# Kernel tuning notes

Hardware: AMD Instinct MI355X
Metric: run time of the kernel (lower is better)

## Reference

```python
import jax, jax.numpy as jnp
import numpy as np

N = 100000          # nodes
E = 1600000         # edges
IN, H, E1, E2, K = 256, 128, 128, 128, 3


def setup_inputs() -> dict:
    key = jax.random.key(0)
    ks = jax.random.split(key, 8)
    s = 0.02
    return {
        "x": jax.random.normal(ks[0], (N, IN), dtype=jnp.float32),
        "edge_index": jax.random.randint(ks[1], (2, E), 0, N),
        "edge_weight": jax.random.uniform(ks[2], (E,), dtype=jnp.float32),
        "W1": jax.random.normal(ks[3], (IN, H), dtype=jnp.float32) * s,
        "b1": jnp.zeros((H,), jnp.float32),
        "cheb1_W": jax.random.normal(ks[4], (K, H, E1), dtype=jnp.float32) * s,
        "cheb1_b": jnp.zeros((E1,), jnp.float32),
        "cheb2_W": jax.random.normal(ks[5], (K, E1, E2), dtype=jnp.float32) * s,
        "cheb2_b": jnp.zeros((E2,), jnp.float32),
        "W2": jax.random.normal(ks[6], (E2, 2), dtype=jnp.float32) * s,
        "b2": jnp.zeros((2,), jnp.float32),
    }


def _cheb_conv(x, row, col, wn, Ws, b):
    """PyG ChebConv with sym normalization, lambda_max=2.
    Scaled Laplacian L_hat = L_sym - I = -D^{-1/2} A D^{-1/2} (zero diagonal),
    so L_hat @ v is a single gather/scale/scatter over edges.
    Tx_0 = x; Tx_1 = L_hat x; Tx_k = 2 L_hat Tx_{k-1} - Tx_{k-2}.
    """
    n = x.shape[0]

    def Lx(v):
        return jax.ops.segment_sum(-wn[:, None] * v[col], row, num_segments=n)

    Tx0 = x
    out = Tx0 @ Ws[0]
    Tx1 = Lx(Tx0)
    out = out + Tx1 @ Ws[1]
    for k in range(2, Ws.shape[0]):
        Tx2 = 2.0 * Lx(Tx1) - Tx0
        out = out + Tx2 @ Ws[k]
        Tx0, Tx1 = Tx1, Tx2
    return out + b


def reference(x, edge_index, edge_weight, W1, b1, cheb1_W, cheb1_b,
              cheb2_W, cheb2_b, W2, b2):
    row, col = edge_index[0], edge_index[1]
    n = x.shape[0]
    # symmetric normalization of edge weights (shared by both convs)
    deg = jax.ops.segment_sum(edge_weight, row, num_segments=n)
    safe = jnp.where(deg > 0, deg, 1.0)
    dinv = jnp.where(deg > 0, jax.lax.rsqrt(safe), 0.0)
    wn = dinv[row] * edge_weight * dinv[col]

    # dropout is identity in eval mode
    h = jax.nn.relu(x @ W1 + b1)
    h = jax.nn.relu(_cheb_conv(h, row, col, wn, cheb1_W, cheb1_b))
    h = jax.nn.relu(_cheb_conv(h, row, col, wn, cheb2_W, cheb2_b))
    logits = h @ W2 + b2
    return jax.nn.softmax(logits, axis=1)
```

## Files before the change

kernel.cpp:

```cpp
#include <hip/hip_runtime.h>
#include <hip/hip_bf16.h>
#include <stdint.h>

typedef __bf16 bf16_t;
typedef __bf16 bf16x8 __attribute__((ext_vector_type(8)));
typedef float f32x4 __attribute__((ext_vector_type(4)));
typedef float f32x2 __attribute__((ext_vector_type(2)));
typedef float floatv4 __attribute__((ext_vector_type(4)));

static __device__ __forceinline__ float bflo(unsigned int p){ return __uint_as_float(p << 16); }
static __device__ __forceinline__ float bfhi(unsigned int p){ return __uint_as_float(p & 0xffff0000u); }
static __device__ __forceinline__ unsigned int pack2(float lo, float hi){
  union { bf16_t h[2]; unsigned int u; } o;
  o.h[0] = (bf16_t)lo; o.h[1] = (bf16_t)hi;
  return o.u;
}
static __device__ __forceinline__ void gload16(const void* g, void* l){
  __builtin_amdgcn_global_load_lds((const __attribute__((address_space(1))) void*)g,
                                   (__attribute__((address_space(3))) void*)l, 16, 0, 0);
}
static __device__ __forceinline__ void acc4_fp8(float* a, unsigned w, float wt){
  f32x2 lo, hi;
  unsigned wh = w >> 16;
  asm("v_cvt_pk_f32_fp8 %0, %1" : "=v"(lo) : "v"(w));
  asm("v_cvt_pk_f32_fp8 %0, %1" : "=v"(hi) : "v"(wh));
  a[0] += wt*lo[0]; a[1] += wt*lo[1]; a[2] += wt*hi[0]; a[3] += wt*hi[1];
}
static __device__ __forceinline__ void dec4_fp8(float* d, unsigned w){
  f32x2 lo, hi;
  unsigned wh = w >> 16;
  asm("v_cvt_pk_f32_fp8 %0, %1" : "=v"(lo) : "v"(w));
  asm("v_cvt_pk_f32_fp8 %0, %1" : "=v"(hi) : "v"(wh));
  d[0] = lo[0]; d[1] = lo[1]; d[2] = hi[0]; d[3] = hi[1];
}
static __device__ __forceinline__ unsigned cvt2fp8(float a, float b){
  unsigned r;
  asm("v_cvt_pk_fp8_f32 %0, %1, %2" : "=v"(r) : "v"(a), "v"(b));
  return r & 0xffffu;
}
static __device__ __forceinline__ uint8_t cvt1fp8(float a){
  unsigned r;
  asm("v_cvt_pk_fp8_f32 %0, %1, %1" : "=v"(r) : "v"(a));
  return (uint8_t)r;
}
static __device__ __forceinline__ unsigned packEdge(int col, float w_pos){
  unsigned b = __float_as_uint(w_pos) + 0x8000u;
  return ((b >> 16) << 17) | (unsigned)col;
}
static __device__ __forceinline__ float edgeWpos(unsigned u){
  return __uint_as_float((u >> 17) << 16);
}
static __device__ __forceinline__ float edgeWneg(unsigned u){
  return __uint_as_float(0x80000000u | ((u >> 17) << 16));
}

constexpr int NN = 100000;
constexpr int NE = 1600000;
constexpr int NB_G  = (NN + 127)/128;
constexpr int NBIN = (NN + 127)/128;
constexpr int EPB  = 4096;
constexpr int NBB  = (NE + EPB - 1)/EPB;
constexpr int MAXBE = 3072;

__global__ __launch_bounds__(256) void k_binA(const int* __restrict__ row,
                                              int* __restrict__ bincnt,
                                              int* __restrict__ blockbase){
  __shared__ int h[NBIN];
  for (int b = threadIdx.x; b < NBIN; b += 256) h[b] = 0;
  __syncthreads();
  int base = blockIdx.x * EPB;
  for (int k = 0; k < EPB; k += 256){
    int i = base + k + threadIdx.x;
    if (i < NE) atomicAdd(&h[row[i] >> 7], 1);
  }
  __syncthreads();
  for (int b = threadIdx.x; b < NBIN; b += 256){
    int c = h[b];
    blockbase[blockIdx.x * NBIN + b] = c ? atomicAdd(&bincnt[b], c) : 0;
  }
}

__global__ __launch_bounds__(256) void k_scanbins(const int* __restrict__ bincnt,
                                                  int* __restrict__ binptr,
                                                  int* __restrict__ rowptr){
  __shared__ int s[256];
  int t = threadIdx.x;
  int b0 = t*4;
  int c[4]; int tot = 0;
  #pragma unroll
  for (int j = 0; j < 4; ++j){
    int b = b0 + j;
    c[j] = (b < NBIN) ? bincnt[b] : 0;
    tot += c[j];
  }
  s[t] = tot;
  __syncthreads();
  for (int off = 1; off < 256; off <<= 1){
    int v = (t >= off) ? s[t - off] : 0;
    __syncthreads();
    s[t] += v;
    __syncthreads();
  }
  int ex = s[t] - tot;
  #pragma unroll
  for (int j = 0; j < 4; ++j){
    int b = b0 + j;
    if (b < NBIN) binptr[b] = ex;
    ex += c[j];
  }
  if (t == 255){ binptr[NBIN] = ex; rowptr[NN] = ex; }
}

__global__ __launch_bounds__(256) void k_binB(const int* __restrict__ row,
                                              const int* __restrict__ col,
                                              const float* __restrict__ w,
                                              const int* __restrict__ binptr,
                                              const int* __restrict__ blockbase,
                                              int2* __restrict__ temp){
  __shared__ int h[NBIN];
  for (int b = threadIdx.x; b < NBIN; b += 256) h[b] = 0;
  __syncthreads();
  int base = blockIdx.x * EPB;
  for (int k = 0; k < EPB; k += 256){
    int i = base + k + threadIdx.x;
    if (i < NE){
      int r = row[i];
      int b = r >> 7;
      int rank = atomicAdd(&h[b], 1);
      int pos = binptr[b] + blockbase[blockIdx.x * NBIN + b] + rank;
      temp[pos] = make_int2(col[i] | ((r & 127) << 17), __float_as_int(w[i]));
    }
  }
}

__global__ __launch_bounds__(256) void k_binC(const int2* __restrict__ temp,
                                              const int* __restrict__ binptr,
                                              unsigned* __restrict__ ec,
                                              int* __restrict__ rowptr,
                                              float* __restrict__ dinv, int n){
  __shared__ int2 sbuf[MAXBE];
  __shared__ int cnt[128];
  __shared__ int scan[128];
  __shared__ int estart[128];
  const int b = blockIdx.x;
  const int e0 = binptr[b];
  int nb = binptr[b+1] - e0; if (nb > MAXBE) nb = MAXBE;
  const int t = threadIdx.x;
  if (t < 128) cnt[t] = 0;
  __syncthreads();
  for (int k = t; k < nb; k += 256)
    atomicAdd(&cnt[(temp[e0+k].x >> 17) & 127], 1);
  __syncthreads();
  if (t < 128) scan[t] = cnt[t];
  __syncthreads();
  for (int off = 1; off < 128; off <<= 1){
    int v = (t < 128 && t >= off) ? scan[t - off] : 0;
    __syncthreads();
    if (t < 128) scan[t] += v;
    __syncthreads();
  }
  if (t < 128){ estart[t] = scan[t] - cnt[t]; cnt[t] = 0; }
  __syncthreads();
  for (int k = t; k < nb; k += 256){
    int2 q = temp[e0+k];
    int rl = (q.x >> 17) & 127;
    int rank = atomicAdd(&cnt[rl], 1);
    sbuf[estart[rl] + rank] = q;
  }
  __syncthreads();
  for (int k = t; k < nb; k += 256){
    int2 q = sbuf[k];
    ec[e0 + k] = packEdge(q.x & 0x1FFFF, __int_as_float(q.y));
  }
  if (t < 128){
    int gid = b*128 + t;
    if (gid < n){
      rowptr[gid] = e0 + estart[t];
      float s = 0.f;
      int s0 = estart[t], c = cnt[t];
      for (int j = 0; j < c; ++j) s += __int_as_float(sbuf[s0+j].y);
      dinv[gid] = (s > 0.f) ? rsqrtf(s) : 0.f;
    }
  }
}

__global__ __launch_bounds__(256) void k_norm(unsigned* __restrict__ ec,
                                              const int* __restrict__ rowptr,
                                              const float* __restrict__ dinv, int n){
  int node = blockIdx.x*4 + (threadIdx.x >> 6);
  if (node >= n) return;
  int lane = threadIdx.x & 63;
  int e0 = rowptr[node], e1 = rowptr[node+1];
  float dr = dinv[node];
  for (int e = e0 + lane; e < e1; e += 64){
    unsigned u = ec[e];
    int c = u & 0x1FFFF;
    float wn = dr * edgeWpos(u) * dinv[c];
    ec[e] = packEdge(c, wn);
  }
}

__global__ void k_transw_all(const float* __restrict__ W1, const float* __restrict__ c1W,
                             const float* __restrict__ c2W, bf16_t* __restrict__ Wt1,
                             uint8_t* __restrict__ W8c1, uint8_t* __restrict__ W8c2){
  int idx = blockIdx.x*256 + threadIdx.x;
  if (idx < 2*16384){
    int c = idx >> 14, r = (idx >> 7) & 127, j = idx & 127;
    Wt1[(c << 14) + (j << 7) + r] = (bf16_t)W1[idx];
  } else if (idx < 5*16384){
    int local = idx - 2*16384;
    int c = local >> 14, r = (local >> 7) & 127, j = local & 127;
    W8c1[(c << 14) + (j << 7) + r] = cvt1fp8(c1W[local]);
  } else {
    int local = idx - 5*16384;
    int c = local >> 14, r = (local >> 7) & 127, j = local & 127;
    W8c2[(c << 14) + (j << 7) + r] = cvt1fp8(c2W[local]);
  }
}

__global__ __launch_bounds__(256) void k_gemm1(
    const float* __restrict__ x, const bf16_t* __restrict__ Wt, const float* __restrict__ bias,
    uint8_t* __restrict__ out8, int M)
{
  __shared__ uint8_t lds[2][16384];
  const int tid = threadIdx.x;
  const int wave = tid >> 6, lane = tid & 63;
  const int wm = wave >> 1, wn = wave & 1;
  const int l15 = lane & 15, lq = lane >> 4;
  const int blockRow = blockIdx.x * 128;
  const int strow = tid >> 3;
  const int scell = tid & 7;

  f32x4 acc[4][4];
  #pragma unroll
  for (int a = 0; a < 4; ++a)
    #pragma unroll
    for (int b = 0; b < 4; ++b) acc[a][b] = f32x4{0.f,0.f,0.f,0.f};

  #pragma unroll
  for (int j = 0; j < 4; ++j){
    int r = j*32 + strow;
    int gr = blockRow + r; if (gr > M-1) gr = M-1;
    gload16((const char*)x + (size_t)gr*1024 + ((scell ^ (r&7)) << 4),
            &lds[0][j*4096 + tid*16]);
  }

  #pragma unroll
  for (int s = 0; s < 8; ++s){
    if (s < 7){
      #pragma unroll
      for (int j = 0; j < 4; ++j){
        int r = j*32 + strow;
        int gr = blockRow + r; if (gr > M-1) gr = M-1;
        gload16((const char*)x + (size_t)gr*1024 + (s+1)*128 + ((scell ^ (r&7)) << 4),
                &lds[(s+1)&1][j*4096 + tid*16]);
      }
    }
    __syncthreads();
    const uint8_t* buf = lds[s&1];
    bf16x8 af[4], bfr[4];
    #pragma unroll
    for (int fm = 0; fm < 4; ++fm){
      int r = wm*64 + fm*16 + l15;
      floatv4 v0 = *(const floatv4*)(buf + r*128 + (((lq*2    ) ^ (r&7)) << 4));
      floatv4 v1 = *(const floatv4*)(buf + r*128 + (((lq*2 + 1) ^ (r&7)) << 4));
      bf16x8 t;
      t[0]=(bf16_t)v0[0]; t[1]=(bf16_t)v0[1]; t[2]=(bf16_t)v0[2]; t[3]=(bf16_t)v0[3];
      t[4]=(bf16_t)v1[0]; t[5]=(bf16_t)v1[1]; t[6]=(bf16_t)v1[2]; t[7]=(bf16_t)v1[3];
      af[fm] = t;
    }
    #pragma unroll
    for (int fn = 0; fn < 4; ++fn)
      bfr[fn] = *(const bf16x8*)(Wt + ((size_t)(((s>>2) << 7) + wn*64 + fn*16 + l15) << 7) + (s&3)*32 + lq*8);
    #pragma unroll
    for (int fm = 0; fm < 4; ++fm)
      #pragma unroll
      for (int fn = 0; fn < 4; ++fn)
        acc[fm][fn] = __builtin_amdgcn_mfma_f32_16x16x32_bf16(af[fm], bfr[fn], acc[fm][fn], 0, 0, 0);
    __syncthreads();
  }
  #pragma unroll
  for (int fm = 0; fm < 4; ++fm){
    #pragma unroll
    for (int j = 0; j < 4; ++j){
      int growo = blockRow + wm*64 + fm*16 + lq*4 + j;
      if (growo < M){
        #pragma unroll
        for (int fn = 0; fn < 4; ++fn){
          int c = wn*64 + fn*16 + l15;
          float v = fmaxf(acc[fm][fn][j] + bias[c], 0.f);
          out8[((size_t)growo << 7) + c] = cvt1fp8(v);
        }
      }
    }
  }
}

__global__ __launch_bounds__(256) void k_gemm8(
    const uint8_t* __restrict__ a0, const uint8_t* __restrict__ a1, const uint8_t* __restrict__ a2,
    const uint8_t* __restrict__ Wt8, const float* __restrict__ bias,
    bf16_t* __restrict__ out, uint8_t* __restrict__ out8, int M)
{
  __shared__ uint8_t lds[2][8192];
  const int tid = threadIdx.x;
  const int wave = tid >> 6, lane = tid & 63;
  const int wm = wave >> 1, wn = wave & 1;
  const int l15 = lane & 15, lq = lane >> 4;
  const int blockRow = blockIdx.x * 128;

  f32x4 acc[4][4];
  #pragma unroll
  for (int a = 0; a < 4; ++a)
    #pragma unroll
    for (int b = 0; b < 4; ++b) acc[a][b] = f32x4{0.f,0.f,0.f,0.f};

  #pragma unroll
  for (int j = 0; j < 2; ++j){
    int flat = j*256 + tid;
    int r = flat >> 2, cell = flat & 3;
    int gr = blockRow + r; if (gr > M-1) gr = M-1;
    gload16(a0 + (size_t)gr*128 + ((cell ^ ((r>>1)&3)) << 4), &lds[0][flat << 4]);
  }

  #pragma unroll
  for (int s = 0; s < 6; ++s){
    if (s < 5){
      const int sn = s + 1;
      const uint8_t* srcn = (sn>>1) == 0 ? a0 : ((sn>>1) == 1 ? a1 : a2);
      #pragma unroll
      for (int j = 0; j < 2; ++j){
        int flat = j*256 + tid;
        int r = flat >> 2, cell = flat & 3;
        int gr = blockRow + r; if (gr > M-1) gr = M-1;
        gload16(srcn + (size_t)gr*128 + (sn&1)*64 + ((cell ^ ((r>>1)&3)) << 4),
                &lds[sn&1][flat << 4]);
      }
    }
    __syncthreads();
    const uint8_t* buf = lds[s&1];
    #pragma unroll
    for (int kk32 = 0; kk32 < 2; ++kk32){
      long af[4], bfr[4];
      #pragma unroll
      for (int fm = 0; fm < 4; ++fm){
        int r = wm*64 + fm*16 + l15;
        int cell = kk32*2 + (lq >> 1);
        af[fm] = *(const long*)(buf + r*64 + ((cell ^ ((r>>1)&3)) << 4) + (lq & 1)*8);
      }
      #pragma unroll
      for (int fn = 0; fn < 4; ++fn)
        bfr[fn] = *(const long*)(Wt8 + ((size_t)(((s>>1) << 7) + wn*64 + fn*16 + l15) << 7)
                                 + (s&1)*64 + kk32*32 + lq*8);
      #pragma unroll
      for (int fm = 0; fm < 4; ++fm)
        #pragma unroll
        for (int fn = 0; fn < 4; ++fn)
          acc[fm][fn] = __builtin_amdgcn_mfma_f32_16x16x32_fp8_fp8(af[fm], bfr[fn], acc[fm][fn], 0, 0, 0);
    }
    __syncthreads();
  }
  #pragma unroll
  for (int fm = 0; fm < 4; ++fm){
    #pragma unroll
    for (int j = 0; j < 4; ++j){
      int growo = blockRow + wm*64 + fm*16 + lq*4 + j;
      if (growo < M){
        #pragma unroll
        for (int fn = 0; fn < 4; ++fn){
          int c = wn*64 + fn*16 + l15;
          float v = fmaxf(acc[fm][fn][j] + bias[c], 0.f);
          if (out)  out[((size_t)growo << 7) + c] = (bf16_t)v;
          if (out8) out8[((size_t)growo << 7) + c] = cvt1fp8(v);
        }
      }
    }
  }
}

__global__ __launch_bounds__(256) void k_spmm8(
    const int* __restrict__ rowptr, const unsigned* __restrict__ ec,
    const uint8_t* __restrict__ V8, const uint8_t* __restrict__ sub8, float alpha,
    uint8_t* __restrict__ out8, int n)
{
  const int lane = threadIdx.x & 63;
  const int wave = threadIdx.x >> 6;
  const int g = lane >> 4;
  const int s = lane & 15;
  const int node = blockIdx.x*16 + wave*4 + g;
  if (node >= n) return;

  int e = rowptr[node];
  const int e1 = rowptr[node+1];
  const int fb = s << 3;

  float acc[8] = {0.f,0.f,0.f,0.f,0.f,0.f,0.f,0.f};

  for (; e + 8 <= e1; e += 8){
    unsigned u0 = ec[e],   u1 = ec[e+1], u2 = ec[e+2], u3 = ec[e+3];
    unsigned u4 = ec[e+4], u5 = ec[e+5], u6 = ec[e+6], u7 = ec[e+7];
    uint2 p0 = *(const uint2*)(V8 + (((size_t)(u0 & 0x1FFFF)) << 7) + fb);
    uint2 p1 = *(const uint2*)(V8 + (((size_t)(u1 & 0x1FFFF)) << 7) + fb);
    uint2 p2 = *(const uint2*)(V8 + (((size_t)(u2 & 0x1FFFF)) << 7) + fb);
    uint2 p3 = *(const uint2*)(V8 + (((size_t)(u3 & 0x1FFFF)) << 7) + fb);
    uint2 p4 = *(const uint2*)(V8 + (((size_t)(u4 & 0x1FFFF)) << 7) + fb);
    uint2 p5 = *(const uint2*)(V8 + (((size_t)(u5 & 0x1FFFF)) << 7) + fb);
    uint2 p6 = *(const uint2*)(V8 + (((size_t)(u6 & 0x1FFFF)) << 7) + fb);
    uint2 p7 = *(const uint2*)(V8 + (((size_t)(u7 & 0x1FFFF)) << 7) + fb);
    float w0 = edgeWneg(u0), w1 = edgeWneg(u1), w2 = edgeWneg(u2), w3 = edgeWneg(u3);
    float w4 = edgeWneg(u4), w5 = edgeWneg(u5), w6 = edgeWneg(u6), w7 = edgeWneg(u7);
    acc4_fp8(acc,   p0.x, w0); acc4_fp8(acc+4, p0.y, w0);
    acc4_fp8(acc,   p1.x, w1); acc4_fp8(acc+4, p1.y, w1);
    acc4_fp8(acc,   p2.x, w2); acc4_fp8(acc+4, p2.y, w2);
    acc4_fp8(acc,   p3.x, w3); acc4_fp8(acc+4, p3.y, w3);
    acc4_fp8(acc,   p4.x, w4); acc4_fp8(acc+4, p4.y, w4);
    acc4_fp8(acc,   p5.x, w5); acc4_fp8(acc+4, p5.y, w5);
    acc4_fp8(acc,   p6.x, w6); acc4_fp8(acc+4, p6.y, w6);
    acc4_fp8(acc,   p7.x, w7); acc4_fp8(acc+4, p7.y, w7);
  }
  for (; e + 4 <= e1; e += 4){
    unsigned u0 = ec[e], u1 = ec[e+1], u2 = ec[e+2], u3 = ec[e+3];
    uint2 p0 = *(const uint2*)(V8 + (((size_t)(u0 & 0x1FFFF)) << 7) + fb);
    uint2 p1 = *(const uint2*)(V8 + (((size_t)(u1 & 0x1FFFF)) << 7) + fb);
    uint2 p2 = *(const uint2*)(V8 + (((size_t)(u2 & 0x1FFFF)) << 7) + fb);
    uint2 p3 = *(const uint2*)(V8 + (((size_t)(u3 & 0x1FFFF)) << 7) + fb);
    float w0 = edgeWneg(u0), w1 = edgeWneg(u1), w2 = edgeWneg(u2), w3 = edgeWneg(u3);
    acc4_fp8(acc,   p0.x, w0); acc4_fp8(acc+4, p0.y, w0);
    acc4_fp8(acc,   p1.x, w1); acc4_fp8(acc+4, p1.y, w1);
    acc4_fp8(acc,   p2.x, w2); acc4_fp8(acc+4, p2.y, w2);
    acc4_fp8(acc,   p3.x, w3); acc4_fp8(acc+4, p3.y, w3);
  }
  for (; e < e1; ++e){
    unsigned u = ec[e];
    uint2 p = *(const uint2*)(V8 + (((size_t)(u & 0x1FFFF)) << 7) + fb);
    float w = edgeWneg(u);
    acc4_fp8(acc, p.x, w); acc4_fp8(acc+4, p.y, w);
  }

  float r[8];
  #pragma unroll
  for (int i = 0; i < 8; ++i) r[i] = alpha*acc[i];
  if (sub8){
    uint2 sv = *(const uint2*)(sub8 + (((size_t)node) << 7) + fb);
    float sd[8];
    dec4_fp8(sd,     sv.x);
    dec4_fp8(sd + 4, sv.y);
    #pragma unroll
    for (int i = 0; i < 8; ++i) r[i] -= sd[i];
  }
  uint2 o8;
  o8.x = cvt2fp8(r[0], r[1]) | (cvt2fp8(r[2], r[3]) << 16);
  o8.y = cvt2fp8(r[4], r[5]) | (cvt2fp8(r[6], r[7]) << 16);
  *(uint2*)(out8 + (((size_t)node) << 7) + fb) = o8;
}

__global__ __launch_bounds__(256) void k_head(
    const bf16_t* __restrict__ h, const float* __restrict__ W2, const float* __restrict__ b2,
    float* __restrict__ out, int n)
{
  int node = blockIdx.x*4 + (threadIdx.x >> 6);
  if (node >= n) return;
  int lane = threadIdx.x & 63;
  unsigned int p = *(const unsigned int*)(h + ((size_t)node << 7) + lane*2);
  float h0 = bflo(p), h1 = bfhi(p);
  floatv4 w = *(const floatv4*)(W2 + lane*4);
  float p0 = h0*w[0] + h1*w[2];
  float p1 = h0*w[1] + h1*w[3];
  #pragma unroll
  for (int s = 32; s > 0; s >>= 1){
    p0 += __shfl_xor(p0, s, 64);
    p1 += __shfl_xor(p1, s, 64);
  }
  if (lane == 0){
    float l0 = p0 + b2[0], l1 = p1 + b2[1];
    float m = fmaxf(l0, l1);
    float e0 = __expf(l0 - m), e1 = __expf(l1 - m);
    float inv = 1.f / (e0 + e1);
    out[(size_t)node*2]     = e0 * inv;
    out[(size_t)node*2 + 1] = e1 * inv;
  }
}


extern "C" void kernel_launch(void* const* d_in, const int* in_sizes, int n_in,
                              void* d_out, int out_size, void* d_ws, size_t ws_size,
                              hipStream_t stream)
{
  const float* x   = (const float*)d_in[0];
  const int*   ei  = (const int*)d_in[1];
  const float* ew  = (const float*)d_in[2];
  const float* W1  = (const float*)d_in[3];
  const float* b1  = (const float*)d_in[4];
  const float* c1W = (const float*)d_in[5];
  const float* c1b = (const float*)d_in[6];
  const float* c2W = (const float*)d_in[7];
  const float* c2b = (const float*)d_in[8];
  const float* W2  = (const float*)d_in[9];
  const float* b2  = (const float*)d_in[10];
  float* out = (float*)d_out;

  const int n = NN, e = NE;
  const int* row = ei;
  const int* col = ei + e;

  char* ws = (char*)d_ws;
  size_t off = 0;
  auto carve = [&](size_t bytes)->void*{
    void* p = ws + off;
    off += (bytes + 255) & ~(size_t)255;
    return p;
  };
  bf16_t*  A   = (bf16_t*)carve((size_t)n*128*2);
  uint8_t* q8a = (uint8_t*)carve((size_t)n*128);
  uint8_t* B8  = (uint8_t*)carve((size_t)n*128);
  uint8_t* C8  = (uint8_t*)carve((size_t)n*128);
  uint8_t* D8  = (uint8_t*)carve((size_t)n*128);
  float*  dinv = (float*)carve((size_t)n*4);
  int*    rowptr = (int*)carve((size_t)(n+1)*4);
  unsigned* ec = (unsigned*)carve((size_t)e*4);
  int*    bincnt = (int*)carve((size_t)NBIN*4);
  int*    binptr = (int*)carve((size_t)(NBIN+1)*4);
  int*    blockbase = (int*)carve((size_t)NBB*NBIN*4);
  bf16_t*  Wt1  = (bf16_t*)carve(2*128*128*2);
  uint8_t* W8c1 = (uint8_t*)carve(3*128*128);
  uint8_t* W8c2 = (uint8_t*)carve(3*128*128);
  int2* temp = (int2*)D8;
  (void)ws_size; (void)in_sizes; (void)n_in; (void)out_size;

  const int NB_W = (n + 3)/4;
  const int NB_S = (n + 15)/16;

  hipMemsetAsync(bincnt, 0, (size_t)NBIN*4, stream);
  k_binA<<<NBB,256,0,stream>>>(row, bincnt, blockbase);
  k_scanbins<<<1,256,0,stream>>>(bincnt, binptr, rowptr);
  k_binB<<<NBB,256,0,stream>>>(row, col, ew, binptr, blockbase, temp);
  k_binC<<<NBIN,256,0,stream>>>(temp, binptr, ec, rowptr, dinv, n);
  k_norm<<<NB_W,256,0,stream>>>(ec, rowptr, dinv, n);
  k_transw_all<<<(8*16384+255)/256,256,0,stream>>>(W1, c1W, c2W, Wt1, W8c1, W8c2);

  k_gemm1<<<NB_G,256,0,stream>>>(x, Wt1, b1, q8a, n);
  k_spmm8<<<NB_S,256,0,stream>>>(rowptr, ec, q8a, nullptr, 1.f, B8, n);
  k_spmm8<<<NB_S,256,0,stream>>>(rowptr, ec, B8, q8a, 2.f, C8, n);
  k_gemm8<<<NB_G,256,0,stream>>>(q8a, B8, C8, W8c1, c1b, nullptr, D8, n);
  k_spmm8<<<NB_S,256,0,stream>>>(rowptr, ec, D8, nullptr, 1.f, B8, n);
  k_spmm8<<<NB_S,256,0,stream>>>(rowptr, ec, B8, D8, 2.f, C8, n);
  k_gemm8<<<NB_G,256,0,stream>>>(D8, B8, C8, W8c2, c2b, A, nullptr, n);
  k_head<<<NB_W,256,0,stream>>>(A, W2, b2, out, n);
}
```

Baseline: 359.7 us.

## Fuse head softmax into last GEMM and merge binning/weight prep into GEMM1

The final output head (h@W2, softmax) now runs in the epilogue of the second ChebConv GEMM, using LDS atomics to reduce logits. This avoids writing and re-reading a 100k x 128 bf16 intermediate and drops one launch. The edge-bin histogram pass and the fp8 weight transposes are packed as extra blocks into the first GEMM launch, so independent work runs concurrently and fewer launches are issued. The cost is a larger LDS footprint in gemm1, which may reduce occupancy, plus shared atomics in the epilogue.

```diff
diff --git a/kernel.cpp b/kernel.cpp
--- a/kernel.cpp
+++ b/kernel.cpp
@@ -8,13 +8,6 @@
 typedef float f32x2 __attribute__((ext_vector_type(2)));
 typedef float floatv4 __attribute__((ext_vector_type(4)));
 
-static __device__ __forceinline__ float bflo(unsigned int p){ return __uint_as_float(p << 16); }
-static __device__ __forceinline__ float bfhi(unsigned int p){ return __uint_as_float(p & 0xffff0000u); }
-static __device__ __forceinline__ unsigned int pack2(float lo, float hi){
-  union { bf16_t h[2]; unsigned int u; } o;
-  o.h[0] = (bf16_t)lo; o.h[1] = (bf16_t)hi;
-  return o.u;
-}
 static __device__ __forceinline__ void gload16(const void* g, void* l){
   __builtin_amdgcn_global_load_lds((const __attribute__((address_space(1))) void*)g,
                                    (__attribute__((address_space(3))) void*)l, 16, 0, 0);
@@ -61,24 +54,7 @@
 constexpr int EPB  = 4096;
 constexpr int NBB  = (NE + EPB - 1)/EPB;
 constexpr int MAXBE = 3072;
-
-__global__ __launch_bounds__(256) void k_binA(const int* __restrict__ row,
-                                              int* __restrict__ bincnt,
-                                              int* __restrict__ blockbase){
-  __shared__ int h[NBIN];
-  for (int b = threadIdx.x; b < NBIN; b += 256) h[b] = 0;
-  __syncthreads();
-  int base = blockIdx.x * EPB;
-  for (int k = 0; k < EPB; k += 256){
-    int i = base + k + threadIdx.x;
-    if (i < NE) atomicAdd(&h[row[i] >> 7], 1);
-  }
-  __syncthreads();
-  for (int b = threadIdx.x; b < NBIN; b += 256){
-    int c = h[b];
-    blockbase[blockIdx.x * NBIN + b] = c ? atomicAdd(&bincnt[b], c) : 0;
-  }
-}
+constexpr int NB_TW8 = (2*3*128*128)/256;
 
 __global__ __launch_bounds__(256) void k_scanbins(const int* __restrict__ bincnt,
                                                   int* __restrict__ binptr,
@@ -200,30 +176,50 @@
   }
 }
 
-__global__ void k_transw_all(const float* __restrict__ W1, const float* __restrict__ c1W,
-                             const float* __restrict__ c2W, bf16_t* __restrict__ Wt1,
-                             uint8_t* __restrict__ W8c1, uint8_t* __restrict__ W8c2){
+__global__ void k_transw1(const float* __restrict__ W1, bf16_t* __restrict__ Wt1){
   int idx = blockIdx.x*256 + threadIdx.x;
-  if (idx < 2*16384){
-    int c = idx >> 14, r = (idx >> 7) & 127, j = idx & 127;
-    Wt1[(c << 14) + (j << 7) + r] = (bf16_t)W1[idx];
-  } else if (idx < 5*16384){
-    int local = idx - 2*16384;
-    int c = local >> 14, r = (local >> 7) & 127, j = local & 127;
-    W8c1[(c << 14) + (j << 7) + r] = cvt1fp8(c1W[local]);
-  } else {
-    int local = idx - 5*16384;
-    int c = local >> 14, r = (local >> 7) & 127, j = local & 127;
-    W8c2[(c << 14) + (j << 7) + r] = cvt1fp8(c2W[local]);
-  }
-}
-
-__global__ __launch_bounds__(256) void k_gemm1(
+  int c = idx >> 14, r = (idx >> 7) & 127, j = idx & 127;
+  Wt1[(c << 14) + (j << 7) + r] = (bf16_t)W1[idx];
+}
+
+__global__ __launch_bounds__(256) void k_gemm1_fused(
     const float* __restrict__ x, const bf16_t* __restrict__ Wt, const float* __restrict__ bias,
-    uint8_t* __restrict__ out8, int M)
+    uint8_t* __restrict__ out8, int M,
+    const int* __restrict__ row, int* __restrict__ bincnt, int* __restrict__ blockbase,
+    const float* __restrict__ c1W, const float* __restrict__ c2W,
+    uint8_t* __restrict__ W8c1, uint8_t* __restrict__ W8c2)
 {
   __shared__ uint8_t lds[2][16384];
+  __shared__ int hA[NBIN];
   const int tid = threadIdx.x;
+
+  if (blockIdx.x >= NB_G + NBB){
+    int base = (blockIdx.x - NB_G - NBB)*256 + tid;
+    int m = base / 49152;
+    int local = base - m*49152;
+    const float* src = m ? c2W : c1W;
+    uint8_t* dst = m ? W8c2 : W8c1;
+    int c = local >> 14, r = (local >> 7) & 127, j = local & 127;
+    dst[(c << 14) + (j << 7) + r] = cvt1fp8(src[local]);
+    return;
+  }
+  if (blockIdx.x >= NB_G){
+    int bb = blockIdx.x - NB_G;
+    for (int b = tid; b < NBIN; b += 256) hA[b] = 0;
+    __syncthreads();
+    int base = bb * EPB;
+    for (int k = 0; k < EPB; k += 256){
+      int i = base + k + tid;
+      if (i < NE) atomicAdd(&hA[row[i] >> 7], 1);
+    }
+    __syncthreads();
+    for (int b = tid; b < NBIN; b += 256){
+      int c = hA[b];
+      blockbase[bb * NBIN + b] = c ? atomicAdd(&bincnt[b], c) : 0;
+    }
+    return;
+  }
+
   const int wave = tid >> 6, lane = tid & 63;
   const int wm = wave >> 1, wn = wave & 1;
   const int l15 = lane & 15, lq = lane >> 4;
@@ -299,9 +295,12 @@
 __global__ __launch_bounds__(256) void k_gemm8(
     const uint8_t* __restrict__ a0, const uint8_t* __restrict__ a1, const uint8_t* __restrict__ a2,
     const uint8_t* __restrict__ Wt8, const float* __restrict__ bias,
-    bf16_t* __restrict__ out, uint8_t* __restrict__ out8, int M)
+    uint8_t* __restrict__ out8,
+    const float* __restrict__ W2h, const float* __restrict__ b2h, float* __restrict__ outh,
+    int M)
 {
   __shared__ uint8_t lds[2][8192];
+  __shared__ float logits[128][2];
   const int tid = threadIdx.x;
   const int wave = tid >> 6, lane = tid & 63;
   const int wm = wave >> 1, wn = wave & 1;
@@ -359,18 +358,61 @@
     }
     __syncthreads();
   }
-  #pragma unroll
-  for (int fm = 0; fm < 4; ++fm){
-    #pragma unroll
-    for (int j = 0; j < 4; ++j){
-      int growo = blockRow + wm*64 + fm*16 + lq*4 + j;
-      if (growo < M){
+
+  if (outh){
+    ((float*)logits)[tid] = 0.f;
+    __syncthreads();
+    float w2l[8];
+    #pragma unroll
+    for (int fn = 0; fn < 4; ++fn){
+      int c = wn*64 + fn*16 + l15;
+      w2l[fn*2]   = W2h[c*2];
+      w2l[fn*2+1] = W2h[c*2+1];
+    }
+    #pragma unroll
+    for (int fm = 0; fm < 4; ++fm){
+      #pragma unroll
+      for (int j = 0; j < 4; ++j){
+        int r = wm*64 + fm*16 + lq*4 + j;
+        int growo = blockRow + r;
+        float p0 = 0.f, p1 = 0.f;
         #pragma unroll
         for (int fn = 0; fn < 4; ++fn){
-          int c = wn*64 + fn*16 + l15;
-          float v = fmaxf(acc[fm][fn][j] + bias[c], 0.f);
-          if (out)  out[((size_t)growo << 7) + c] = (bf16_t)v;
-          if (out8) out8[((size_t)growo << 7) + c] = cvt1fp8(v);
+          float v = fmaxf(acc[fm][fn][j] + bias[wn*64 + fn*16 + l15], 0.f);
+          p0 += v*w2l[fn*2];
+          p1 += v*w2l[fn*2+1];
+        }
+        if (growo < M){
+          atomicAdd(&logits[r][0], p0);
+          atomicAdd(&logits[r][1], p1);
+        }
+      }
+    }
+    __syncthreads();
+    if (tid < 128){
+      int node = blockRow + tid;
+      if (node < M){
+        float l0 = logits[tid][0] + b2h[0];
+        float l1 = logits[tid][1] + b2h[1];
+        float mx = fmaxf(l0, l1);
+        float e0 = __expf(l0 - mx), e1 = __expf(l1 - mx);
+        float inv = 1.f / (e0 + e1);
+        *(float2*)(outh + (size_t)node*2) = make_float2(e0*inv, e1*inv);
+      }
+    }
+  } else {
+    #pragma unroll
+    for (int fm = 0; fm < 4; ++fm){
+      #pragma unroll
+      for (int j = 0; j < 4; ++j){
+        int growo = blockRow + wm*64 + fm*16 + lq*4 + j;
+        if (growo < M){
+          #pragma unroll
+          for (int fn = 0; fn < 4; ++fn){
+            int c = wn*64 + fn*16 + l15;
+            float v = fmaxf(acc[fm][fn][j] + bias[c], 0.f);
+            out8[((size_t)growo << 7) + c] = cvt1fp8(v);
+          }
         }
       }
     }
@@ -453,33 +495,6 @@
   *(uint2*)(out8 + (((size_t)node) << 7) + fb) = o8;
 }
 
-__global__ __launch_bounds__(256) void k_head(
-    const bf16_t* __restrict__ h, const float* __restrict__ W2, const float* __restrict__ b2,
-    float* __restrict__ out, int n)
-{
-  int node = blockIdx.x*4 + (threadIdx.x >> 6);
-  if (node >= n) return;
-  int lane = threadIdx.x & 63;
-  unsigned int p = *(const unsigned int*)(h + ((size_t)node << 7) + lane*2);
-  float h0 = bflo(p), h1 = bfhi(p);
-  floatv4 w = *(const floatv4*)(W2 + lane*4);
-  float p0 = h0*w[0] + h1*w[2];
-  float p1 = h0*w[1] + h1*w[3];
-  #pragma unroll
-  for (int s = 32; s > 0; s >>= 1){
-    p0 += __shfl_xor(p0, s, 64);
-    p1 += __shfl_xor(p1, s, 64);
-  }
-  if (lane == 0){
-    float l0 = p0 + b2[0], l1 = p1 + b2[1];
-    float m = fmaxf(l0, l1);
-    float e0 = __expf(l0 - m), e1 = __expf(l1 - m);
-    float inv = 1.f / (e0 + e1);
-    out[(size_t)node*2]     = e0 * inv;
-    out[(size_t)node*2 + 1] = e1 * inv;
-  }
-}
-
 
 extern "C" void kernel_launch(void* const* d_in, const int* in_sizes, int n_in,
                               void* d_out, int out_size, void* d_ws, size_t ws_size,
@@ -509,7 +524,6 @@
     off += (bytes + 255) & ~(size_t)255;
     return p;
   };
-  bf16_t*  A   = (bf16_t*)carve((size_t)n*128*2);
   uint8_t* q8a = (uint8_t*)carve((size_t)n*128);
   uint8_t* B8  = (uint8_t*)carve((size_t)n*128);
   uint8_t* C8  = (uint8_t*)carve((size_t)n*128);
@@ -530,19 +544,18 @@
   const int NB_S = (n + 15)/16;
 
   hipMemsetAsync(bincnt, 0, (size_t)NBIN*4, stream);
-  k_binA<<<NBB,256,0,stream>>>(row, bincnt, blockbase);
+  k_transw1<<<128,256,0,stream>>>(W1, Wt1);
+  k_gemm1_fused<<<NB_G + NBB + NB_TW8,256,0,stream>>>(
+      x, Wt1, b1, q8a, n, row, bincnt, blockbase, c1W, c2W, W8c1, W8c2);
   k_scanbins<<<1,256,0,stream>>>(bincnt, binptr, rowptr);
   k_binB<<<NBB,256,0,stream>>>(row, col, ew, binptr, blockbase, temp);
   k_binC<<<NBIN,256,0,stream>>>(temp, binptr, ec, rowptr, dinv, n);
   k_norm<<<NB_W,256,0,stream>>>(ec, rowptr, dinv, n);
-  k_transw_all<<<(8*16384+255)/256,256,0,stream>>>(W1, c1W, c2W, Wt1, W8c1, W8c2);
-
-  k_gemm1<<<NB_G,256,0,stream>>>(x, Wt1, b1, q8a, n);
+
   k_spmm8<<<NB_S,256,0,stream>>>(rowptr, ec, q8a, nullptr, 1.f, B8, n);
   k_spmm8<<<NB_S,256,0,stream>>>(rowptr, ec, B8, q8a, 2.f, C8, n);
-  k_gemm8<<<NB_G,256,0,stream>>>(q8a, B8, C8, W8c1, c1b, nullptr, D8, n);
+  k_gemm8<<<NB_G,256,0,stream>>>(q8a, B8, C8, W8c1, c1b, D8, nullptr, nullptr, nullptr, n);
   k_spmm8<<<NB_S,256,0,stream>>>(rowptr, ec, D8, nullptr, 1.f, B8, n);
   k_spmm8<<<NB_S,256,0,stream>>>(rowptr, ec, B8, D8, 2.f, C8, n);
-  k_gemm8<<<NB_G,256,0,stream>>>(D8, B8, C8, W8c2, c2b, A, nullptr, n);
-  k_head<<<NB_W,256,0,stream>>>(A, W2, b2, out, n);
-}
+  k_gemm8<<<NB_G,256,0,stream>>>(D8, B8, C8, W8c2, c2b, nullptr, W2, b2, out, n);
+}
```

New measurement: 352.1 us. -2.1%, faster.
